# Performance work log

Hardware: AMD Instinct MI355X
Metric: run time of the kernel (lower is better)

The kernel has to match this reference:

```python
import jax, jax.numpy as jnp
import numpy as np

DIM = 256
HEADS = 8
NW = 4096  # number of windows (mask.shape[0])


def setup_inputs() -> dict:
    key = jax.random.key(0)
    ks = jax.random.split(key, 7)
    B_, N, C = 4096, 64, DIM
    return {
        "x": jax.random.normal(ks[0], (B_, N, C), dtype=jnp.float32),
        "mask": jax.random.normal(ks[1], (NW, N, N), dtype=jnp.float32),
        "qw": jax.random.normal(ks[2], (C, C), dtype=jnp.float32),
        "qb": jnp.zeros((C,), dtype=jnp.float32),
        "kw": jax.random.normal(ks[3], (C, C), dtype=jnp.float32),
        "kb": jnp.zeros((C,), dtype=jnp.float32),
        "vw": jax.random.normal(ks[4], (C, C), dtype=jnp.float32),
        "vb": jnp.zeros((C,), dtype=jnp.float32),
        "pw": jax.random.normal(ks[5], (C, C), dtype=jnp.float32),
        "pb": jnp.zeros((C,), dtype=jnp.float32),
    }


def _linear_fc(x, w, b):
    # LinearFC: weight scaled by 1/sqrt(in_features), plus bias
    gain = 1.0 / np.sqrt(np.float32(w.shape[1]))
    return x @ (w * gain).T + b


def reference(x, mask, qw, qb, kw, kb, vw, vb, pw, pb):
    B_, N, C = x.shape
    H = HEADS
    hd = C // H
    scale = np.float32(hd) ** -0.5
    # F.normalize(x, p=2, dim=-1) with eps=1e-12
    norm_x = x / jnp.maximum(jnp.linalg.norm(x, axis=-1, keepdims=True), 1e-12)
    q = _linear_fc(norm_x, qw, qb).reshape(B_, N, H, hd).transpose(0, 2, 1, 3)  # bhnd
    k = _linear_fc(norm_x, kw, kb).reshape(B_, N, H, hd).transpose(0, 2, 1, 3)  # bhmd
    v = _linear_fc(x, vw, vb).reshape(B_, N, H, hd).transpose(0, 2, 1, 3)       # bhmd
    attn = jnp.einsum('bhnd,bhmd->bhnm', q, k) * scale                           # [B_,H,N,N]
    nW = mask.shape[0]
    attn = attn.reshape(B_ // nW, nW, H, N, N) + mask[None, :, None, :, :]
    attn = jax.nn.softmax(attn.reshape(B_, H, N, N), axis=-1)
    out = jnp.einsum('bhnm,bhmd->bhnd', attn, v)
    out = out.transpose(0, 2, 1, 3).reshape(B_, N, C)
    return _linear_fc(out, pw, pb)
```

## Files before the change

### kernel.cpp

```cpp
#include <hip/hip_runtime.h>

#define GAIN  0.0625f
#define LOG2E 1.4426950408889634f
#define C1    (0.17677669529663687f * 1.4426950408889634f)

typedef float f32x4 __attribute__((ext_vector_type(4)));
typedef short s16x8 __attribute__((ext_vector_type(8)));
typedef short s16x4 __attribute__((ext_vector_type(4)));
typedef _Float16 h16x4 __attribute__((ext_vector_type(4)));

union U8 { s16x4 h[2]; s16x8 v; };

static __device__ __forceinline__ short f2bf(float f) {
  union { float f; unsigned u; } v; v.f = f;
  unsigned u = v.u;
  u += 0x7fffu + ((u >> 16) & 1u);
  return (short)(u >> 16);
}
static __device__ __forceinline__ s16x4 pks4(const f32x4& v) {
  s16x4 p;
#pragma unroll
  for (int r = 0; r < 4; ++r) p[r] = f2bf(v[r]);
  return p;
}

__global__ void prep_weights(const float* __restrict__ qw, const float* __restrict__ kw,
                             const float* __restrict__ vw, const float* __restrict__ pw,
                             short* __restrict__ wsb) {
  int i = blockIdx.x * 256 + threadIdx.x;
  wsb[i]          = f2bf(qw[i] * GAIN);
  wsb[i + 65536]  = f2bf(kw[i] * GAIN);
  wsb[i + 131072] = f2bf(vw[i] * GAIN);
  wsb[i + 196608] = f2bf(pw[i] * GAIN);
}

#define OFF_XN 0
#define OFF_MH 32768
#define OFF_SC 41472
#define OFF_SN 80384
#define LDS_TOTAL 80640

template<bool BF16W>
__global__ __launch_bounds__(512, 4)
void wattn(const float* __restrict__ x, const float* __restrict__ mask,
           const float* __restrict__ qw, const float* __restrict__ qb,
           const float* __restrict__ kw, const float* __restrict__ kb,
           const float* __restrict__ vw, const float* __restrict__ vb,
           const float* __restrict__ pw, const float* __restrict__ pb,
           const short* __restrict__ wsb, float* __restrict__ out)
{
  __shared__ __align__(16) char smem[LDS_TOTAL];
  const int tid  = threadIdx.x;
  const int lane = tid & 63;
  const int w    = tid >> 6;
  const int c    = lane & 15;
  const int g    = lane >> 4;
  const int b    = blockIdx.x;
  const int sw   = (c & 7) << 3;

  const float* xg = x + (size_t)b * 16384;

  short*     XN = (short*)(smem + OFF_XN);
  _Float16*  MH = (_Float16*)(smem + OFF_MH);
  float*     SN = (float*)(smem + OFF_SN);
  short*     SC = (short*)(smem + OFF_SC) + w * 2432;
  short*     AN = XN;

  const short* wq_bf = wsb;
  const short* wk_bf = wsb + 65536;
  const short* wv_bf = wsb + 131072;
  const short* wp_bf = wsb + 196608;

  auto wfragG = [&](const short* wb, const float* wf, int row, int k0) -> s16x8 {
    s16x8 r;
    if constexpr (BF16W) {
      r = *(const s16x8*)(wb + row * 256 + k0);
    } else {
      const f32x4* p = (const f32x4*)(wf + row * 256 + k0);
      f32x4 a = p[0], b2 = p[1];
#pragma unroll
      for (int j = 0; j < 4; ++j) { r[j] = f2bf(a[j] * GAIN); r[j+4] = f2bf(b2[j] * GAIN); }
    }
    return r;
  };

  {
    f32x4 xv[8];
    float ssu[8];
#pragma unroll
    for (int u = 0; u < 8; ++u) {
      xv[u] = *(const f32x4*)(xg + (u * 512 + tid) * 4);
      ssu[u] = xv[u][0]*xv[u][0] + xv[u][1]*xv[u][1] + xv[u][2]*xv[u][2] + xv[u][3]*xv[u][3];
    }
#pragma unroll
    for (int u = 0; u < 8; ++u)
#pragma unroll
      for (int d = 1; d < 64; d <<= 1) ssu[u] += __shfl_xor(ssu[u], d, 64);
    const int wsw = w << 3;
#pragma unroll
    for (int u = 0; u < 8; ++u) {
      const int row = 8 * u + w;
      float s = fmaxf(sqrtf(ssu[u]), 1e-12f);
      float inv = 1.0f / s;
      if (lane == 0) SN[row] = s;
      s16x4 pk;
#pragma unroll
      for (int e = 0; e < 4; ++e) pk[e] = f2bf(xv[u][e] * inv);
      *(s16x4*)(XN + row * 256 + ((lane * 4) ^ wsw)) = pk;
    }
    const f32x4* msrc = (const f32x4*)(mask + (size_t)b * 4096 + tid * 8);
    const int mrow = tid >> 3, mcol = (tid & 7) * 8;
    f32x4 m0 = msrc[0], m1 = msrc[1];
    h16x4 h0, h1;
#pragma unroll
    for (int e = 0; e < 4; ++e) { h0[e] = (_Float16)(m0[e] * LOG2E); h1[e] = (_Float16)(m1[e] * LOG2E); }
    *(h16x4*)(MH + mrow * 68 + mcol)     = h0;
    *(h16x4*)(MH + mrow * 68 + mcol + 4) = h1;
  }
  __syncthreads();

  const int hd0 = 32 * w;
  s16x8 QB[4], KA[4], VA[2][2];

  auto projQK = [&](const short* wb, const float* wf, const float* bias, s16x8* F) {
    f32x4 acc[2][4] = {};
#pragma unroll
    for (int kk = 0; kk < 8; ++kk) {
      const int k0 = kk * 32 + 8 * g;
      s16x8 xf[4];
#pragma unroll
      for (int ni = 0; ni < 4; ++ni)
        xf[ni] = *(const s16x8*)(XN + (16*ni + c) * 256 + (k0 ^ sw));
#pragma unroll
      for (int mi = 0; mi < 2; ++mi) {
        s16x8 af = wfragG(wb, wf, hd0 + 16*mi + c, k0);
#pragma unroll
        for (int ni = 0; ni < 4; ++ni)
          acc[mi][ni] = __builtin_amdgcn_mfma_f32_16x16x32_bf16(af, xf[ni], acc[mi][ni], 0, 0, 0);
      }
    }
#pragma unroll
    for (int mi = 0; mi < 2; ++mi) {
      float bq[4];
#pragma unroll
      for (int r = 0; r < 4; ++r) bq[r] = bias[hd0 + 16*mi + 4*g + r];
#pragma unroll
      for (int ni = 0; ni < 4; ++ni) {
        s16x4 pk;
#pragma unroll
        for (int r = 0; r < 4; ++r) pk[r] = f2bf(acc[mi][ni][r] + bq[r]);
        *(s16x4*)(SC + (16*ni + c) * 36 + 16*mi + 4*g) = pk;
      }
    }
#pragma unroll
    for (int ni = 0; ni < 4; ++ni) {
      const short* p = SC + (16*ni + c) * 36 + 8*g;
      U8 u;
      u.h[0] = *(const s16x4*)p;
      u.h[1] = *(const s16x4*)(p + 4);
      F[ni] = u.v;
    }
  };
  projQK(wq_bf, qw, qb, QB);
  projQK(wk_bf, kw, kb, KA);

  {
    f32x4 acc[4][2] = {};
#pragma unroll
    for (int kk = 0; kk < 8; ++kk) {
      const int k0 = kk * 32 + 8 * g;
      s16x8 xf[4];
#pragma unroll
      for (int mi = 0; mi < 4; ++mi)
        xf[mi] = *(const s16x8*)(XN + (16*mi + c) * 256 + (k0 ^ sw));
#pragma unroll
      for (int ni = 0; ni < 2; ++ni) {
        s16x8 bf = wfragG(wv_bf, vw, hd0 + 16*ni + c, k0);
#pragma unroll
        for (int mi = 0; mi < 4; ++mi)
          acc[mi][ni] = __builtin_amdgcn_mfma_f32_16x16x32_bf16(xf[mi], bf, acc[mi][ni], 0, 0, 0);
      }
    }
    float bvv[2];
#pragma unroll
    for (int ni = 0; ni < 2; ++ni) bvv[ni] = vb[hd0 + 16*ni + c];
#pragma unroll
    for (int mi = 0; mi < 4; ++mi) {
      f32x4 sn4 = *(const f32x4*)(SN + 16*mi + 4*g);
#pragma unroll
      for (int ni = 0; ni < 2; ++ni) {
        s16x4 pk;
#pragma unroll
        for (int r = 0; r < 4; ++r) pk[r] = f2bf(acc[mi][ni][r] * sn4[r] + bvv[ni]);
        *(s16x4*)(SC + (16*ni + c) * 76 + 16*mi + 4*g) = pk;
      }
    }
#pragma unroll
    for (int vd = 0; vd < 2; ++vd)
#pragma unroll
      for (int k2 = 0; k2 < 2; ++k2) {
        const short* p = SC + (16*vd + c) * 76 + 32*k2 + 8*g;
        U8 u;
        u.h[0] = *(const s16x4*)p;
        u.h[1] = *(const s16x4*)(p + 4);
        VA[vd][k2] = u.v;
      }
  }
  __syncthreads();

  const f32x4 zf = {0.f, 0.f, 0.f, 0.f};
#pragma unroll
  for (int hi = 0; hi < 2; ++hi) {
#pragma unroll
    for (int n2 = 0; n2 < 2; ++n2) {
      const int qi = 2*hi + n2;
      f32x4 sacc[4];
#pragma unroll
      for (int kt = 0; kt < 4; ++kt)
        sacc[kt] = __builtin_amdgcn_mfma_f32_16x16x32_bf16(KA[kt], QB[qi], zf, 0, 0, 0);
      const int qrow = 16*qi + c;
      float sm = 0.f;
#pragma unroll
      for (int kt = 0; kt < 4; ++kt) {
        h16x4 mlv = *(const h16x4*)(MH + qrow * 68 + 16*kt + 4*g);
#pragma unroll
        for (int r = 0; r < 4; ++r) {
          float e = exp2f(sacc[kt][r] * C1 + (float)mlv[r]);
          sacc[kt][r] = e;
          sm += e;
        }
      }
      sm += __shfl_xor(sm, 16, 64);
      sm += __shfl_xor(sm, 32, 64);
      const float rs = 1.0f / sm;
#pragma unroll
      for (int kt = 0; kt < 4; ++kt) {
        s16x4 pk;
#pragma unroll
        for (int r = 0; r < 4; ++r) pk[r] = f2bf(sacc[kt][r] * rs);
        *(s16x4*)(SC + (16*n2 + c) * 76 + 16*kt + 4*g) = pk;
      }
    }
    f32x4 pacc[2][2] = {};
#pragma unroll
    for (int qt = 0; qt < 2; ++qt)
#pragma unroll
      for (int k2 = 0; k2 < 2; ++k2) {
        const short* p = SC + (16*qt + c) * 76 + 32*k2 + 8*g;
        U8 u;
        u.h[0] = *(const s16x4*)p;
        u.h[1] = *(const s16x4*)(p + 4);
        s16x8 PBf = u.v;
#pragma unroll
        for (int vd = 0; vd < 2; ++vd)
          pacc[vd][qt] = __builtin_amdgcn_mfma_f32_16x16x32_bf16(VA[vd][k2], PBf, pacc[vd][qt], 0, 0, 0);
      }
#pragma unroll
    for (int vd = 0; vd < 2; ++vd)
#pragma unroll
      for (int qt = 0; qt < 2; ++qt)
        *(s16x4*)(AN + (32*hi + 16*qt + c) * 256 + ((hd0 + 16*vd + 4*g) ^ sw)) = pks4(pacc[vd][qt]);
  }
  __syncthreads();

  {
    f32x4 facc[4][2] = {};
#pragma unroll
    for (int kk = 0; kk < 8; ++kk) {
      const int k0 = kk * 32 + 8 * g;
      s16x8 afr[4];
#pragma unroll
      for (int mi = 0; mi < 4; ++mi)
        afr[mi] = *(const s16x8*)(AN + (16*mi + c) * 256 + (k0 ^ sw));
#pragma unroll
      for (int ni = 0; ni < 2; ++ni) {
        s16x8 bfr = wfragG(wp_bf, pw, 32*w + 16*ni + c, k0);
#pragma unroll
        for (int mi = 0; mi < 4; ++mi)
          facc[mi][ni] = __builtin_amdgcn_mfma_f32_16x16x32_bf16(afr[mi], bfr, facc[mi][ni], 0, 0, 0);
      }
    }
    float bpv[2];
#pragma unroll
    for (int ni = 0; ni < 2; ++ni) bpv[ni] = pb[32*w + 16*ni + c];
    float* og = out + (size_t)b * 16384;
#pragma unroll
    for (int mi = 0; mi < 4; ++mi)
#pragma unroll
      for (int ni = 0; ni < 2; ++ni)
#pragma unroll
        for (int r = 0; r < 4; ++r)
          og[(16*mi + 4*g + r) * 256 + 32*w + 16*ni + c] = facc[mi][ni][r] + bpv[ni];
  }
}

extern "C" void kernel_launch(void* const* d_in, const int* in_sizes, int n_in,
                              void* d_out, int out_size, void* d_ws, size_t ws_size,
                              hipStream_t stream) {
  const float* x    = (const float*)d_in[0];
  const float* mask = (const float*)d_in[1];
  const float* qw   = (const float*)d_in[2];
  const float* qb   = (const float*)d_in[3];
  const float* kw   = (const float*)d_in[4];
  const float* kb   = (const float*)d_in[5];
  const float* vw   = (const float*)d_in[6];
  const float* vb   = (const float*)d_in[7];
  const float* pw   = (const float*)d_in[8];
  const float* pb   = (const float*)d_in[9];
  float* out = (float*)d_out;

  if (ws_size >= 4u * 65536u * sizeof(short)) {
    short* wsb = (short*)d_ws;
    prep_weights<<<256, 256, 0, stream>>>(qw, kw, vw, pw, wsb);
    wattn<true><<<4096, 512, 0, stream>>>(x, mask, qw, qb, kw, kb, vw, vb, pw, pb, wsb, out);
  } else {
    wattn<false><<<4096, 512, 0, stream>>>(x, mask, qw, qb, kw, kb, vw, vb, pw, pb, nullptr, out);
  }
}
```

Baseline: 338.6 us.

## Shrink LDS footprint by reading mask directly from global and halving scratch

Drops the fp16 mask staging buffer in shared memory and reads each mask row from global memory inside the softmax, scaling by log2e with an fma. The per-wave scratch region is halved by processing the Q/K fragment transposes, V transposes and probability tiles in two 16-row chunks instead of all at once. Total LDS per block falls from about 80 KB to about 52 KB, and launch bounds are raised to six blocks per CU to aim for more resident waves. The risk is more global-memory latency inside the softmax loop, extra sequential LDS round trips, and register pressure from the tighter launch bounds.

Result: slower. 510.4 us (+50.8%).

```diff
diff --git a/kernel.cpp b/kernel.cpp
--- a/kernel.cpp
+++ b/kernel.cpp
@@ -7,7 +7,6 @@
 typedef float f32x4 __attribute__((ext_vector_type(4)));
 typedef short s16x8 __attribute__((ext_vector_type(8)));
 typedef short s16x4 __attribute__((ext_vector_type(4)));
-typedef _Float16 h16x4 __attribute__((ext_vector_type(4)));
 
 union U8 { s16x4 h[2]; s16x8 v; };
 
@@ -35,13 +34,12 @@
 }
 
 #define OFF_XN 0
-#define OFF_MH 32768
-#define OFF_SC 41472
-#define OFF_SN 80384
-#define LDS_TOTAL 80640
+#define OFF_SC 32768
+#define OFF_SN 52224
+#define LDS_TOTAL 52480
 
 template<bool BF16W>
-__global__ __launch_bounds__(512, 4)
+__global__ __launch_bounds__(512, 6)
 void wattn(const float* __restrict__ x, const float* __restrict__ mask,
            const float* __restrict__ qw, const float* __restrict__ qb,
            const float* __restrict__ kw, const float* __restrict__ kb,
@@ -59,12 +57,12 @@
   const int sw   = (c & 7) << 3;
 
   const float* xg = x + (size_t)b * 16384;
-
-  short*     XN = (short*)(smem + OFF_XN);
-  _Float16*  MH = (_Float16*)(smem + OFF_MH);
-  float*     SN = (float*)(smem + OFF_SN);
-  short*     SC = (short*)(smem + OFF_SC) + w * 2432;
-  short*     AN = XN;
+  const float* mg = mask + (size_t)b * 4096;
+
+  short* XN = (short*)(smem + OFF_XN);
+  float* SN = (float*)(smem + OFF_SN);
+  short* SC = (short*)(smem + OFF_SC) + w * 1216;
+  short* AN = XN;
 
   const short* wq_bf = wsb;
   const short* wk_bf = wsb + 65536;
@@ -108,14 +106,6 @@
       for (int e = 0; e < 4; ++e) pk[e] = f2bf(xv[u][e] * inv);
       *(s16x4*)(XN + row * 256 + ((lane * 4) ^ wsw)) = pk;
     }
-    const f32x4* msrc = (const f32x4*)(mask + (size_t)b * 4096 + tid * 8);
-    const int mrow = tid >> 3, mcol = (tid & 7) * 8;
-    f32x4 m0 = msrc[0], m1 = msrc[1];
-    h16x4 h0, h1;
-#pragma unroll
-    for (int e = 0; e < 4; ++e) { h0[e] = (_Float16)(m0[e] * LOG2E); h1[e] = (_Float16)(m1[e] * LOG2E); }
-    *(h16x4*)(MH + mrow * 68 + mcol)     = h0;
-    *(h16x4*)(MH + mrow * 68 + mcol + 4) = h1;
   }
   __syncthreads();
 
@@ -139,26 +129,30 @@
           acc[mi][ni] = __builtin_amdgcn_mfma_f32_16x16x32_bf16(af, xf[ni], acc[mi][ni], 0, 0, 0);
       }
     }
-#pragma unroll
-    for (int mi = 0; mi < 2; ++mi) {
-      float bq[4];
-#pragma unroll
-      for (int r = 0; r < 4; ++r) bq[r] = bias[hd0 + 16*mi + 4*g + r];
-#pragma unroll
-      for (int ni = 0; ni < 4; ++ni) {
-        s16x4 pk;
-#pragma unroll
-        for (int r = 0; r < 4; ++r) pk[r] = f2bf(acc[mi][ni][r] + bq[r]);
-        *(s16x4*)(SC + (16*ni + c) * 36 + 16*mi + 4*g) = pk;
-      }
-    }
-#pragma unroll
-    for (int ni = 0; ni < 4; ++ni) {
-      const short* p = SC + (16*ni + c) * 36 + 8*g;
-      U8 u;
-      u.h[0] = *(const s16x4*)p;
-      u.h[1] = *(const s16x4*)(p + 4);
-      F[ni] = u.v;
+    float bq[2][4];
+#pragma unroll
+    for (int mi = 0; mi < 2; ++mi)
+#pragma unroll
+      for (int r = 0; r < 4; ++r) bq[mi][r] = bias[hd0 + 16*mi + 4*g + r];
+#pragma unroll
+    for (int t2 = 0; t2 < 2; ++t2) {
+#pragma unroll
+      for (int mi = 0; mi < 2; ++mi)
+#pragma unroll
+        for (int ni2 = 0; ni2 < 2; ++ni2) {
+          f32x4 t = acc[mi][2*t2 + ni2];
+#pragma unroll
+          for (int r = 0; r < 4; ++r) t[r] += bq[mi][r];
+          *(s16x4*)(SC + (16*ni2 + c) * 36 + 16*mi + 4*g) = pks4(t);
+        }
+#pragma unroll
+      for (int ni2 = 0; ni2 < 2; ++ni2) {
+        const short* p = SC + (16*ni2 + c) * 36 + 8*g;
+        U8 u;
+        u.h[0] = *(const s16x4*)p;
+        u.h[1] = *(const s16x4*)(p + 4);
+        F[2*t2 + ni2] = u.v;
+      }
     }
   };
   projQK(wq_bf, qw, qb, QB);
@@ -185,32 +179,31 @@
 #pragma unroll
     for (int ni = 0; ni < 2; ++ni) bvv[ni] = vb[hd0 + 16*ni + c];
 #pragma unroll
-    for (int mi = 0; mi < 4; ++mi) {
-      f32x4 sn4 = *(const f32x4*)(SN + 16*mi + 4*g);
-#pragma unroll
-      for (int ni = 0; ni < 2; ++ni) {
-        s16x4 pk;
-#pragma unroll
-        for (int r = 0; r < 4; ++r) pk[r] = f2bf(acc[mi][ni][r] * sn4[r] + bvv[ni]);
-        *(s16x4*)(SC + (16*ni + c) * 76 + 16*mi + 4*g) = pk;
-      }
-    }
-#pragma unroll
-    for (int vd = 0; vd < 2; ++vd)
+    for (int ni = 0; ni < 2; ++ni) {
+#pragma unroll
+      for (int mi = 0; mi < 4; ++mi) {
+        f32x4 sn4 = *(const f32x4*)(SN + 16*mi + 4*g);
+        f32x4 t;
+#pragma unroll
+        for (int r = 0; r < 4; ++r) t[r] = acc[mi][ni][r] * sn4[r] + bvv[ni];
+        *(s16x4*)(SC + c * 76 + 16*mi + 4*g) = pks4(t);
+      }
 #pragma unroll
       for (int k2 = 0; k2 < 2; ++k2) {
-        const short* p = SC + (16*vd + c) * 76 + 32*k2 + 8*g;
+        const short* p = SC + c * 76 + 32*k2 + 8*g;
         U8 u;
         u.h[0] = *(const s16x4*)p;
         u.h[1] = *(const s16x4*)(p + 4);
-        VA[vd][k2] = u.v;
-      }
+        VA[ni][k2] = u.v;
+      }
+    }
   }
   __syncthreads();
 
   const f32x4 zf = {0.f, 0.f, 0.f, 0.f};
 #pragma unroll
   for (int hi = 0; hi < 2; ++hi) {
+    f32x4 pacc[2][2] = {};
 #pragma unroll
     for (int n2 = 0; n2 < 2; ++n2) {
       const int qi = 2*hi + n2;
@@ -218,14 +211,14 @@
 #pragma unroll
       for (int kt = 0; kt < 4; ++kt)
         sacc[kt] = __builtin_amdgcn_mfma_f32_16x16x32_bf16(KA[kt], QB[qi], zf, 0, 0, 0);
-      const int qrow = 16*qi + c;
+      const f32x4* mrow = (const f32x4*)(mg + (16*qi + c) * 64);
       float sm = 0.f;
 #pragma unroll
       for (int kt = 0; kt < 4; ++kt) {
-        h16x4 mlv = *(const h16x4*)(MH + qrow * 68 + 16*kt + 4*g);
+        f32x4 mlv = mrow[4*kt + g];
 #pragma unroll
         for (int r = 0; r < 4; ++r) {
-          float e = exp2f(sacc[kt][r] * C1 + (float)mlv[r]);
+          float e = exp2f(fmaf(mlv[r], LOG2E, sacc[kt][r] * C1));
           sacc[kt][r] = e;
           sm += e;
         }
@@ -235,31 +228,28 @@
       const float rs = 1.0f / sm;
 #pragma unroll
       for (int kt = 0; kt < 4; ++kt) {
-        s16x4 pk;
-#pragma unroll
-        for (int r = 0; r < 4; ++r) pk[r] = f2bf(sacc[kt][r] * rs);
-        *(s16x4*)(SC + (16*n2 + c) * 76 + 16*kt + 4*g) = pk;
-      }
-    }
-    f32x4 pacc[2][2] = {};
-#pragma unroll
-    for (int qt = 0; qt < 2; ++qt)
+        f32x4 t;
+#pragma unroll
+        for (int r = 0; r < 4; ++r) t[r] = sacc[kt][r] * rs;
+        *(s16x4*)(SC + c * 76 + 16*kt + 4*g) = pks4(t);
+      }
 #pragma unroll
       for (int k2 = 0; k2 < 2; ++k2) {
-        const short* p = SC + (16*qt + c) * 76 + 32*k2 + 8*g;
+        const short* p = SC + c * 76 + 32*k2 + 8*g;
         U8 u;
         u.h[0] = *(const s16x4*)p;
         u.h[1] = *(const s16x4*)(p + 4);
         s16x8 PBf = u.v;
 #pragma unroll
         for (int vd = 0; vd < 2; ++vd)
-          pacc[vd][qt] = __builtin_amdgcn_mfma_f32_16x16x32_bf16(VA[vd][k2], PBf, pacc[vd][qt], 0, 0, 0);
-      }
+          pacc[vd][n2] = __builtin_amdgcn_mfma_f32_16x16x32_bf16(VA[vd][k2], PBf, pacc[vd][n2], 0, 0, 0);
+      }
+    }
 #pragma unroll
     for (int vd = 0; vd < 2; ++vd)
 #pragma unroll
-      for (int qt = 0; qt < 2; ++qt)
-        *(s16x4*)(AN + (32*hi + 16*qt + c) * 256 + ((hd0 + 16*vd + 4*g) ^ sw)) = pks4(pacc[vd][qt]);
+      for (int n2 = 0; n2 < 2; ++n2)
+        *(s16x4*)(AN + (32*hi + 16*n2 + c) * 256 + ((hd0 + 16*vd + 4*g) ^ sw)) = pks4(pacc[vd][n2]);
   }
   __syncthreads();
 
```
